# Kernel optimization log

Hardware: AMD Instinct MI355X
Metric: run time of the kernel (lower is better)

Reference implementation:

```python
import jax, jax.numpy as jnp
import numpy as np

DIM = 1024
HEADS = 16
DIM_HEAD = 64
NUM_KV_HEADS = 4
INNER = HEADS * DIM_HEAD          # 1024
KV_DIM = NUM_KV_HEADS * DIM_HEAD  # 256
SCALE = DIM_HEAD ** -0.5


def setup_inputs() -> dict:
    key = jax.random.key(0)
    ks = jax.random.split(key, 7)
    B, S = 2, 2048
    x = jax.random.normal(ks[0], (B, S, DIM), dtype=jnp.float32)
    init = lambda k, shape: jax.random.normal(k, shape, dtype=jnp.float32) * (shape[0] ** -0.5)
    return {
        "x": x,
        "ln_gamma": jnp.ones((DIM,), jnp.float32),
        "ln_beta": jnp.zeros((DIM,), jnp.float32),
        "w_q": init(ks[1], (DIM, INNER)),
        "w_k": init(ks[2], (DIM, KV_DIM)),
        "w_v": init(ks[3], (DIM, KV_DIM)),
        "w_o": init(ks[4], (INNER, DIM)),
        "b_o": jnp.zeros((DIM,), jnp.float32),
    }


def reference(x, ln_gamma, ln_beta, w_q, w_k, w_v, w_o, b_o):
    B, S, _ = x.shape
    g, hpg, d = NUM_KV_HEADS, HEADS // NUM_KV_HEADS, DIM_HEAD
    # LayerNorm (eps matches torch default 1e-5)
    mu = jnp.mean(x, axis=-1, keepdims=True)
    var = jnp.mean((x - mu) ** 2, axis=-1, keepdims=True)
    xn = (x - mu) * jax.lax.rsqrt(var + 1e-5) * ln_gamma + ln_beta
    # projections
    q = xn @ w_q  # [B,S,INNER]
    k = xn @ w_k  # [B,S,KV_DIM]
    v = xn @ w_v
    # q: b s (g hpg d) -> b g hpg s d  (head index h = g*hpg + i, g-major)
    q = q.reshape(B, S, g, hpg, d).transpose(0, 2, 3, 1, 4)
    k = k.reshape(B, S, g, d).transpose(0, 2, 1, 3)  # [B,g,S,d]
    v = v.reshape(B, S, g, d).transpose(0, 2, 1, 3)
    dots = jnp.einsum('bghqd,bgkd->bghqk', q, k) * SCALE
    attn = jax.nn.softmax(dots, axis=-1)
    out = jnp.einsum('bghqk,bgkd->bghqd', attn, v)
    # b g hpg s d -> b s (g hpg d)
    out = out.transpose(0, 3, 1, 2, 4).reshape(B, S, INNER)
    return out @ w_o + b_o
```

## Files before the change

kernel.cpp:

```cpp
#include <hip/hip_runtime.h>

typedef unsigned short u16;
typedef __bf16 bf16x8 __attribute__((ext_vector_type(8)));
typedef short s16x4 __attribute__((ext_vector_type(4)));
typedef float f32x4 __attribute__((ext_vector_type(4)));

__device__ __forceinline__ unsigned f2u(float f) { union { float f; unsigned u; } v; v.f = f; return v.u; }
__device__ __forceinline__ float u2f(unsigned u) { union { unsigned u; float f; } v; v.u = u; return v.f; }

__device__ __forceinline__ u16 f32_to_bf16(float f) {
  unsigned u = f2u(f);
  return (u16)((u + 0x7FFFu + ((u >> 16) & 1u)) >> 16);
}
__device__ __forceinline__ unsigned pack_rnd(float a, float b) {
  unsigned ra = f2u(a), rb = f2u(b);
  ra = ra + 0x7FFFu + ((ra >> 16) & 1u);
  rb = (rb + 0x7FFFu + ((rb >> 16) & 1u)) & 0xFFFF0000u;
  return (ra >> 16) | rb;
}
__device__ __forceinline__ unsigned pack_trunc(float a, float b) {
#if __has_builtin(__builtin_amdgcn_perm)
  return __builtin_amdgcn_perm(f2u(b), f2u(a), 0x07060302u);
#else
  return (f2u(a) >> 16) | (f2u(b) & 0xFFFF0000u);
#endif
}
__device__ __forceinline__ unsigned perm_lo(unsigned a, unsigned b) {
#if __has_builtin(__builtin_amdgcn_perm)
  return __builtin_amdgcn_perm(b, a, 0x05040100u);
#else
  return (a & 0xFFFFu) | (b << 16);
#endif
}
__device__ __forceinline__ unsigned perm_hi(unsigned a, unsigned b) {
#if __has_builtin(__builtin_amdgcn_perm)
  return __builtin_amdgcn_perm(b, a, 0x07060302u);
#else
  return (a >> 16) | (b & 0xFFFF0000u);
#endif
}

__global__ __launch_bounds__(256) void transpose_cvt_multi(
    const float* __restrict__ w_q, const float* __restrict__ w_k,
    const float* __restrict__ w_v, const float* __restrict__ w_o,
    u16* __restrict__ wqkvT, u16* __restrict__ woT) {
  const float* src; u16* dst; int N;
  switch (blockIdx.z) {
    case 0: src = w_q; dst = wqkvT; N = 1024; break;
    case 1: src = w_k; dst = wqkvT + 1024 * 1024; N = 256; break;
    case 2: src = w_v; dst = wqkvT + 1280 * 1024; N = 256; break;
    default: src = w_o; dst = woT; N = 1024; break;
  }
  int n0 = blockIdx.x * 64;
  if (n0 >= N) return;
  const int K = 1024;
  __shared__ float tile[64][65];
  int k0 = blockIdx.y * 64;
  int t = threadIdx.x;
  int c = t & 63, r4 = t >> 6;
#pragma unroll
  for (int rr = r4; rr < 64; rr += 4)
    tile[rr][c] = src[(size_t)(k0 + rr) * N + n0 + c];
  __syncthreads();
#pragma unroll
  for (int rr = r4; rr < 64; rr += 4)
    dst[(size_t)(n0 + rr) * K + k0 + c] = f32_to_bf16(tile[c][rr]);
}

__global__ __launch_bounds__(256) void ln_kernel(
    const float* __restrict__ x, const float* __restrict__ gamma,
    const float* __restrict__ beta, u16* __restrict__ xn) {
  int row = blockIdx.x;
  int t = threadIdx.x;
  const float4 v = ((const float4*)(x + (size_t)row * 1024))[t];
  float s = v.x + v.y + v.z + v.w;
  float ss = v.x * v.x + v.y * v.y + v.z * v.z + v.w * v.w;
#pragma unroll
  for (int m = 1; m < 64; m <<= 1) {
    s += __shfl_xor(s, m, 64);
    ss += __shfl_xor(ss, m, 64);
  }
  __shared__ float as_[4], ass[4];
  int wave = t >> 6;
  if ((t & 63) == 0) { as_[wave] = s; ass[wave] = ss; }
  __syncthreads();
  s = as_[0] + as_[1] + as_[2] + as_[3];
  ss = ass[0] + ass[1] + ass[2] + ass[3];
  float mu = s * (1.0f / 1024.0f);
  float var = ss * (1.0f / 1024.0f) - mu * mu;
  float rstd = rsqrtf(var + 1e-5f);
  float4 g = ((const float4*)gamma)[t];
  float4 b = ((const float4*)beta)[t];
  uint2 o;
  o.x = pack_rnd((v.x - mu) * rstd * g.x + b.x, (v.y - mu) * rstd * g.y + b.y);
  o.y = pack_rnd((v.z - mu) * rstd * g.z + b.z, (v.w - mu) * rstd * g.w + b.w);
  ((uint2*)(xn + (size_t)row * 1024))[t] = o;
}

template <int OUT_MODE>
__global__ __launch_bounds__(256) void gemm_bf16_k(
    const u16* __restrict__ A, const u16* __restrict__ Bt,
    void* __restrict__ Cv, const float* __restrict__ bias,
    int M, int N, int K, int ldc, float qscale, int qcols) {
  __shared__ __align__(16) u16 sA[64 * 72];
  __shared__ __align__(16) u16 sB[128 * 72];
  int t = threadIdx.x;
  int m0 = blockIdx.y * 64, n0 = blockIdx.x * 128;
  int wave = t >> 6, lane = t & 63;
  int wm = wave >> 1, wn = wave & 1;
  int l15 = lane & 15, quad = lane >> 4;

  f32x4 acc[2][4];
#pragma unroll
  for (int i = 0; i < 2; i++)
#pragma unroll
    for (int j = 0; j < 4; j++) acc[i][j] = f32x4{0.f, 0.f, 0.f, 0.f};

  int r = t >> 3, q = t & 7;
  const u16* Ap = A + (size_t)(m0 + r) * K + q * 8;
  const u16* Bp = Bt + (size_t)(n0 + r) * K + q * 8;

  for (int k0 = 0; k0 < K; k0 += 64) {
    uint4 av0 = *(const uint4*)(Ap + k0);
    uint4 av1 = *(const uint4*)(Ap + k0 + (size_t)32 * K);
    uint4 bv0 = *(const uint4*)(Bp + k0);
    uint4 bv1 = *(const uint4*)(Bp + k0 + (size_t)32 * K);
    uint4 bv2 = *(const uint4*)(Bp + k0 + (size_t)64 * K);
    uint4 bv3 = *(const uint4*)(Bp + k0 + (size_t)96 * K);
    __syncthreads();
    *(uint4*)&sA[(r) * 72 + q * 8] = av0;
    *(uint4*)&sA[(r + 32) * 72 + q * 8] = av1;
    *(uint4*)&sB[(r) * 72 + q * 8] = bv0;
    *(uint4*)&sB[(r + 32) * 72 + q * 8] = bv1;
    *(uint4*)&sB[(r + 64) * 72 + q * 8] = bv2;
    *(uint4*)&sB[(r + 96) * 72 + q * 8] = bv3;
    __syncthreads();
#pragma unroll
    for (int ks = 0; ks < 2; ++ks) {
      bf16x8 af[2], bf[4];
#pragma unroll
      for (int mi = 0; mi < 2; mi++)
        af[mi] = *(const bf16x8*)&sA[(wm * 32 + mi * 16 + l15) * 72 + ks * 32 + quad * 8];
#pragma unroll
      for (int ni = 0; ni < 4; ni++)
        bf[ni] = *(const bf16x8*)&sB[(wn * 64 + ni * 16 + l15) * 72 + ks * 32 + quad * 8];
#pragma unroll
      for (int mi = 0; mi < 2; mi++)
#pragma unroll
        for (int ni = 0; ni < 4; ni++)
          acc[mi][ni] = __builtin_amdgcn_mfma_f32_16x16x32_bf16(
              af[mi], bf[ni], acc[mi][ni], 0, 0, 0);
    }
  }
#pragma unroll
  for (int mi = 0; mi < 2; mi++)
#pragma unroll
    for (int ni = 0; ni < 4; ni++) {
      int row = m0 + wm * 32 + mi * 16 + quad * 4;
      int col = n0 + wn * 64 + ni * 16 + l15;
#pragma unroll
      for (int rr = 0; rr < 4; rr++) {
        float vv = acc[mi][ni][rr];
        if (OUT_MODE == 0) {
          float sc = (col < qcols) ? qscale : 1.0f;
          ((u16*)Cv)[(size_t)(row + rr) * ldc + col] = f32_to_bf16(vv * sc);
        } else {
          ((float*)Cv)[(size_t)(row + rr) * ldc + col] = vv + bias[col];
        }
      }
    }
}

__global__ __launch_bounds__(256) void attn_kernel(
    const u16* __restrict__ qkv, u16* __restrict__ oP0, u16* __restrict__ oP1,
    float* __restrict__ lP0, float* __restrict__ lP1) {
  const int LD = 1536;
  int qt = blockIdx.x;
  int bh = blockIdx.y;
  int kz = blockIdx.z;
  int b = bh >> 4, h = bh & 15, g = h >> 2;
  u16* oP = kz ? oP1 : oP0;
  float* lP = kz ? lP1 : lP0;

  __shared__ __align__(16) u16 sK[64 * 72];
  __shared__ __align__(16) u16 sV[64 * 72];

  int t = threadIdx.x, wave = t >> 6, lane = t & 63;
  int l15 = lane & 15, quad = lane >> 4;

  const u16* qbase = qkv + (size_t)(b * 2048 + qt * 256 + wave * 64) * LD + h * 64;
  const u16* kbase = qkv + (size_t)(b * 2048 + kz * 1024) * LD + 1024 + g * 64;
  const u16* vbase = kbase + 256;

  bf16x8 qf[4][2];
#pragma unroll
  for (int qs = 0; qs < 4; ++qs)
#pragma unroll
    for (int ks = 0; ks < 2; ++ks)
      qf[qs][ks] = *(const bf16x8*)(qbase + (size_t)(qs * 16 + l15) * LD + ks * 32 + quad * 8);

  f32x4 oacc[4][4];
  f32x4 lacc[4];
#pragma unroll
  for (int qs = 0; qs < 4; ++qs) {
    lacc[qs] = f32x4{0.f, 0.f, 0.f, 0.f};
#pragma unroll
    for (int md = 0; md < 4; ++md) oacc[qs][md] = f32x4{0.f, 0.f, 0.f, 0.f};
  }

  const s16x4 ones = {(short)0x3F80, (short)0x3F80, (short)0x3F80, (short)0x3F80};
  const f32x4 fzero = {0.f, 0.f, 0.f, 0.f};

  int sr = t >> 3, sq = t & 7;
  int vkp = (t & 31) * 2, vdc = (t >> 5) * 8;

  uint4 ka0, ka1, va0, va1;
  {
    const u16* kp0 = kbase + (size_t)sr * LD + sq * 8;
    ka0 = *(const uint4*)kp0;
    ka1 = *(const uint4*)(kp0 + (size_t)32 * LD);
    const u16* vp0 = vbase + (size_t)vkp * LD + vdc;
    va0 = *(const uint4*)vp0;
    va1 = *(const uint4*)(vp0 + LD);
  }

  for (int kt = 0; kt < 16; ++kt) {
    __syncthreads();
    *(uint4*)&sK[sr * 72 + sq * 8] = ka0;
    *(uint4*)&sK[(sr + 32) * 72 + sq * 8] = ka1;
    {
      const unsigned* aw = (const unsigned*)&va0;
      const unsigned* bw = (const unsigned*)&va1;
#pragma unroll
      for (int w = 0; w < 4; ++w) {
        *(unsigned*)&sV[(vdc + 2 * w) * 72 + vkp] = perm_lo(aw[w], bw[w]);
        *(unsigned*)&sV[(vdc + 2 * w + 1) * 72 + vkp] = perm_hi(aw[w], bw[w]);
      }
    }
    __syncthreads();

    if (kt < 15) {
      const u16* kp0 = kbase + (size_t)((kt + 1) * 64 + sr) * LD + sq * 8;
      ka0 = *(const uint4*)kp0;
      ka1 = *(const uint4*)(kp0 + (size_t)32 * LD);
      const u16* vp0 = vbase + (size_t)((kt + 1) * 64 + vkp) * LD + vdc;
      va0 = *(const uint4*)vp0;
      va1 = *(const uint4*)(vp0 + LD);
    }

    s16x4 pf[4][4];
#pragma unroll
    for (int ni = 0; ni < 4; ++ni) {
      bf16x8 kf0 = *(const bf16x8*)&sK[(ni * 16 + l15) * 72 + quad * 8];
      bf16x8 kf1 = *(const bf16x8*)&sK[(ni * 16 + l15) * 72 + 32 + quad * 8];
      f32x4 sacc[4];
#pragma unroll
      for (int qs = 0; qs < 4; ++qs)
        sacc[qs] = __builtin_amdgcn_mfma_f32_16x16x32_bf16(kf0, qf[qs][0], fzero, 0, 0, 0);
#pragma unroll
      for (int qs = 0; qs < 4; ++qs)
        sacc[qs] = __builtin_amdgcn_mfma_f32_16x16x32_bf16(kf1, qf[qs][1], sacc[qs], 0, 0, 0);
#pragma unroll
      for (int qs = 0; qs < 4; ++qs) {
        float p0 = __builtin_amdgcn_exp2f(sacc[qs][0]);
        float p1 = __builtin_amdgcn_exp2f(sacc[qs][1]);
        float p2 = __builtin_amdgcn_exp2f(sacc[qs][2]);
        float p3 = __builtin_amdgcn_exp2f(sacc[qs][3]);
        uint2 pk;
        pk.x = pack_trunc(p0, p1);
        pk.y = pack_trunc(p2, p3);
        pf[qs][ni] = *(s16x4*)&pk;
        lacc[qs] = __builtin_amdgcn_mfma_f32_16x16x16bf16_1k(ones, pf[qs][ni], lacc[qs], 0, 0, 0);
      }
    }

#pragma unroll
    for (int md = 0; md < 4; ++md)
#pragma unroll
      for (int ni = 0; ni < 4; ++ni) {
        s16x4 vf = *(const s16x4*)&sV[(md * 16 + l15) * 72 + ni * 16 + quad * 4];
#pragma unroll
        for (int qs = 0; qs < 4; ++qs)
          oacc[qs][md] = __builtin_amdgcn_mfma_f32_16x16x16bf16_1k(vf, pf[qs][ni], oacc[qs][md], 0, 0, 0);
      }
  }

#pragma unroll
  for (int qs = 0; qs < 4; ++qs) {
    int row = b * 2048 + qt * 256 + wave * 64 + qs * 16 + l15;
    u16* ob = oP + (size_t)row * 1024 + h * 64 + quad * 4;
#pragma unroll
    for (int md = 0; md < 4; ++md) {
      uint2 o;
      o.x = pack_rnd(oacc[qs][md][0], oacc[qs][md][1]);
      o.y = pack_rnd(oacc[qs][md][2], oacc[qs][md][3]);
      *(uint2*)(ob + md * 16) = o;
    }
    if (quad == 0) lP[row * 16 + h] = lacc[qs][0];
  }
}

__global__ __launch_bounds__(256) void attn_combine(
    const u16* __restrict__ oP0, u16* __restrict__ oP1_attn,
    const float* __restrict__ lP0, const float* __restrict__ lP1) {
  int t = threadIdx.x;
  int row = blockIdx.x * 2 + (t >> 7);
  int c8 = (t & 127) * 8;
  int h = c8 >> 6;
  float l = lP0[row * 16 + h] + lP1[row * 16 + h];
  float rinv = 1.0f / l;
  size_t off = (size_t)row * 1024 + c8;
  uint4 a = *(const uint4*)(oP0 + off);
  uint4 bb = *(const uint4*)(oP1_attn + off);
  const unsigned* aw = (const unsigned*)&a;
  const unsigned* bw = (const unsigned*)&bb;
  uint4 o;
  unsigned* ow = (unsigned*)&o;
#pragma unroll
  for (int i = 0; i < 4; ++i) {
    float x0 = u2f(aw[i] << 16) + u2f(bw[i] << 16);
    float x1 = u2f(aw[i] & 0xFFFF0000u) + u2f(bw[i] & 0xFFFF0000u);
    ow[i] = pack_rnd(x0 * rinv, x1 * rinv);
  }
  *(uint4*)(oP1_attn + off) = o;
}

extern "C" void kernel_launch(void* const* d_in, const int* in_sizes, int n_in,
                              void* d_out, int out_size, void* d_ws, size_t ws_size,
                              hipStream_t stream) {
  const float* x = (const float*)d_in[0];
  const float* gamma = (const float*)d_in[1];
  const float* beta = (const float*)d_in[2];
  const float* w_q = (const float*)d_in[3];
  const float* w_k = (const float*)d_in[4];
  const float* w_v = (const float*)d_in[5];
  const float* w_o = (const float*)d_in[6];
  const float* b_o = (const float*)d_in[7];
  float* out = (float*)d_out;

  char* ws = (char*)d_ws;
  u16* wqkvT = (u16*)ws;
  float* lP0 = (float*)ws;
  float* lP1 = (float*)(ws + 256u * 1024);
  u16* woT = (u16*)(ws + 3u * 1024 * 1024);
  u16* xn = (u16*)(ws + 5u * 1024 * 1024);
  u16* oP0 = xn;
  u16* qkv = (u16*)(ws + 13u * 1024 * 1024);
  u16* oP1 = (u16*)(ws + 25u * 1024 * 1024);

  const float cexp = 0.125f * 1.44269504088896f;

  transpose_cvt_multi<<<dim3(16, 16, 4), 256, 0, stream>>>(w_q, w_k, w_v, w_o,
                                                           wqkvT, woT);
  ln_kernel<<<4096, 256, 0, stream>>>(x, gamma, beta, xn);

  gemm_bf16_k<0><<<dim3(12, 64), 256, 0, stream>>>(xn, wqkvT, qkv, nullptr,
                                                   4096, 1536, 1024, 1536,
                                                   cexp, 1024);

  attn_kernel<<<dim3(8, 32, 2), 256, 0, stream>>>(qkv, oP0, oP1, lP0, lP1);
  attn_combine<<<dim3(2048), 256, 0, stream>>>(oP0, oP1, lP0, lP1);

  gemm_bf16_k<1><<<dim3(8, 64), 256, 0, stream>>>(oP1, woT, out, b_o,
                                                  4096, 1024, 1024, 1024,
                                                  1.0f, 0);
}
```

Before: 187.3 us.

## Switch attention inner loops to 32x32x16 bf16 MFMA tiles

Rewrites the attention kernel's QK^T, PV and row-sum accumulation to use 32x32x16 bf16 MFMA instructions instead of 16x16 variants. The P fragments produced by the score MFMA feed the PV MFMA directly, and the V tile is stored to shared memory with a permuted key-column index so its layout matches the 32x32 operand layout. The aim is fewer MFMA issues and fewer LDS fragment loads per tile. In exchange it needs larger accumulator register sets (f32x16), which raises register pressure and may lower occupancy.

```diff
diff --git a/kernel.cpp b/kernel.cpp
--- a/kernel.cpp
+++ b/kernel.cpp
@@ -4,6 +4,7 @@
 typedef __bf16 bf16x8 __attribute__((ext_vector_type(8)));
 typedef short s16x4 __attribute__((ext_vector_type(4)));
 typedef float f32x4 __attribute__((ext_vector_type(4)));
+typedef float f32x16 __attribute__((ext_vector_type(16)));
 
 __device__ __forceinline__ unsigned f2u(float f) { union { float f; unsigned u; } v; v.f = f; return v.u; }
 __device__ __forceinline__ float u2f(unsigned u) { union { unsigned u; float f; } v; v.u = u; return v.f; }
@@ -186,33 +187,35 @@
   __shared__ __align__(16) u16 sV[64 * 72];
 
   int t = threadIdx.x, wave = t >> 6, lane = t & 63;
-  int l15 = lane & 15, quad = lane >> 4;
+  int l31 = lane & 31, hh = lane >> 5;
 
   const u16* qbase = qkv + (size_t)(b * 2048 + qt * 256 + wave * 64) * LD + h * 64;
   const u16* kbase = qkv + (size_t)(b * 2048 + kz * 1024) * LD + 1024 + g * 64;
   const u16* vbase = kbase + 256;
 
-  bf16x8 qf[4][2];
-#pragma unroll
-  for (int qs = 0; qs < 4; ++qs)
-#pragma unroll
-    for (int ks = 0; ks < 2; ++ks)
-      qf[qs][ks] = *(const bf16x8*)(qbase + (size_t)(qs * 16 + l15) * LD + ks * 32 + quad * 8);
-
-  f32x4 oacc[4][4];
-  f32x4 lacc[4];
-#pragma unroll
-  for (int qs = 0; qs < 4; ++qs) {
-    lacc[qs] = f32x4{0.f, 0.f, 0.f, 0.f};
-#pragma unroll
-    for (int md = 0; md < 4; ++md) oacc[qs][md] = f32x4{0.f, 0.f, 0.f, 0.f};
-  }
-
-  const s16x4 ones = {(short)0x3F80, (short)0x3F80, (short)0x3F80, (short)0x3F80};
-  const f32x4 fzero = {0.f, 0.f, 0.f, 0.f};
+  bf16x8 qf[2][4];
+#pragma unroll
+  for (int q2 = 0; q2 < 2; ++q2)
+#pragma unroll
+    for (int ds = 0; ds < 4; ++ds)
+      qf[q2][ds] = *(const bf16x8*)(qbase + (size_t)(q2 * 32 + l31) * LD + ds * 16 + hh * 8);
+
+  f32x16 oacc[2][2];
+  f32x16 lacc[2];
+#pragma unroll
+  for (int i = 0; i < 16; ++i) {
+    oacc[0][0][i] = 0.f; oacc[0][1][i] = 0.f;
+    oacc[1][0][i] = 0.f; oacc[1][1][i] = 0.f;
+    lacc[0][i] = 0.f; lacc[1][i] = 0.f;
+  }
+  union { u16 s[8]; bf16x8 v; } vones;
+#pragma unroll
+  for (int i = 0; i < 8; ++i) vones.s[i] = 0x3F80;
 
   int sr = t >> 3, sq = t & 7;
   int vkp = (t & 31) * 2, vdc = (t >> 5) * 8;
+  int x = vkp & 15;
+  int vc = (vkp & ~15) | (x & 3) | ((x & 4) << 1) | ((x & 8) >> 1);
 
   uint4 ka0, ka1, va0, va1;
   {
@@ -233,8 +236,8 @@
       const unsigned* bw = (const unsigned*)&va1;
 #pragma unroll
       for (int w = 0; w < 4; ++w) {
-        *(unsigned*)&sV[(vdc + 2 * w) * 72 + vkp] = perm_lo(aw[w], bw[w]);
-        *(unsigned*)&sV[(vdc + 2 * w + 1) * 72 + vkp] = perm_hi(aw[w], bw[w]);
+        *(unsigned*)&sV[(vdc + 2 * w) * 72 + vc] = perm_lo(aw[w], bw[w]);
+        *(unsigned*)&sV[(vdc + 2 * w + 1) * 72 + vc] = perm_hi(aw[w], bw[w]);
       }
     }
     __syncthreads();
@@ -248,55 +251,69 @@
       va1 = *(const uint4*)(vp0 + LD);
     }
 
-    s16x4 pf[4][4];
-#pragma unroll
-    for (int ni = 0; ni < 4; ++ni) {
-      bf16x8 kf0 = *(const bf16x8*)&sK[(ni * 16 + l15) * 72 + quad * 8];
-      bf16x8 kf1 = *(const bf16x8*)&sK[(ni * 16 + l15) * 72 + 32 + quad * 8];
-      f32x4 sacc[4];
-#pragma unroll
-      for (int qs = 0; qs < 4; ++qs)
-        sacc[qs] = __builtin_amdgcn_mfma_f32_16x16x32_bf16(kf0, qf[qs][0], fzero, 0, 0, 0);
-#pragma unroll
-      for (int qs = 0; qs < 4; ++qs)
-        sacc[qs] = __builtin_amdgcn_mfma_f32_16x16x32_bf16(kf1, qf[qs][1], sacc[qs], 0, 0, 0);
-#pragma unroll
-      for (int qs = 0; qs < 4; ++qs) {
-        float p0 = __builtin_amdgcn_exp2f(sacc[qs][0]);
-        float p1 = __builtin_amdgcn_exp2f(sacc[qs][1]);
-        float p2 = __builtin_amdgcn_exp2f(sacc[qs][2]);
-        float p3 = __builtin_amdgcn_exp2f(sacc[qs][3]);
-        uint2 pk;
-        pk.x = pack_trunc(p0, p1);
-        pk.y = pack_trunc(p2, p3);
-        pf[qs][ni] = *(s16x4*)&pk;
-        lacc[qs] = __builtin_amdgcn_mfma_f32_16x16x16bf16_1k(ones, pf[qs][ni], lacc[qs], 0, 0, 0);
-      }
-    }
-
-#pragma unroll
-    for (int md = 0; md < 4; ++md)
-#pragma unroll
-      for (int ni = 0; ni < 4; ++ni) {
-        s16x4 vf = *(const s16x4*)&sV[(md * 16 + l15) * 72 + ni * 16 + quad * 4];
-#pragma unroll
-        for (int qs = 0; qs < 4; ++qs)
-          oacc[qs][md] = __builtin_amdgcn_mfma_f32_16x16x16bf16_1k(vf, pf[qs][ni], oacc[qs][md], 0, 0, 0);
-      }
-  }
-
-#pragma unroll
-  for (int qs = 0; qs < 4; ++qs) {
-    int row = b * 2048 + qt * 256 + wave * 64 + qs * 16 + l15;
-    u16* ob = oP + (size_t)row * 1024 + h * 64 + quad * 4;
-#pragma unroll
-    for (int md = 0; md < 4; ++md) {
-      uint2 o;
-      o.x = pack_rnd(oacc[qs][md][0], oacc[qs][md][1]);
-      o.y = pack_rnd(oacc[qs][md][2], oacc[qs][md][3]);
-      *(uint2*)(ob + md * 16) = o;
-    }
-    if (quad == 0) lP[row * 16 + h] = lacc[qs][0];
+#pragma unroll
+    for (int ktile = 0; ktile < 2; ++ktile) {
+      bf16x8 kf[4];
+#pragma unroll
+      for (int ds = 0; ds < 4; ++ds)
+        kf[ds] = *(const bf16x8*)&sK[(ktile * 32 + l31) * 72 + ds * 16 + hh * 8];
+
+      union { unsigned u[4]; bf16x8 v; } pb[2][2];
+#pragma unroll
+      for (int q2 = 0; q2 < 2; ++q2) {
+        f32x16 sc;
+#pragma unroll
+        for (int i = 0; i < 16; ++i) sc[i] = 0.f;
+#pragma unroll
+        for (int ds = 0; ds < 4; ++ds)
+          sc = __builtin_amdgcn_mfma_f32_32x32x16_bf16(kf[ds], qf[q2][ds], sc, 0, 0, 0);
+        unsigned p[8];
+#pragma unroll
+        for (int i = 0; i < 8; ++i) {
+          float e0 = __builtin_amdgcn_exp2f(sc[2 * i]);
+          float e1 = __builtin_amdgcn_exp2f(sc[2 * i + 1]);
+          p[i] = pack_trunc(e0, e1);
+        }
+        pb[q2][0].u[0] = p[0]; pb[q2][0].u[1] = p[1];
+        pb[q2][0].u[2] = p[2]; pb[q2][0].u[3] = p[3];
+        pb[q2][1].u[0] = p[4]; pb[q2][1].u[1] = p[5];
+        pb[q2][1].u[2] = p[6]; pb[q2][1].u[3] = p[7];
+      }
+
+#pragma unroll
+      for (int u = 0; u < 2; ++u) {
+        int s = ktile * 2 + u;
+#pragma unroll
+        for (int dt = 0; dt < 2; ++dt) {
+          bf16x8 vf = *(const bf16x8*)&sV[(dt * 32 + l31) * 72 + s * 16 + hh * 8];
+#pragma unroll
+          for (int q2 = 0; q2 < 2; ++q2)
+            oacc[q2][dt] = __builtin_amdgcn_mfma_f32_32x32x16_bf16(
+                vf, pb[q2][u].v, oacc[q2][dt], 0, 0, 0);
+        }
+#pragma unroll
+        for (int q2 = 0; q2 < 2; ++q2)
+          lacc[q2] = __builtin_amdgcn_mfma_f32_32x32x16_bf16(
+              vones.v, pb[q2][u].v, lacc[q2], 0, 0, 0);
+      }
+    }
+  }
+
+#pragma unroll
+  for (int q2 = 0; q2 < 2; ++q2) {
+    int row = b * 2048 + qt * 256 + wave * 64 + q2 * 32 + l31;
+    if (hh == 0) lP[row * 16 + h] = lacc[q2][0];
+    u16* ob = oP + (size_t)row * 1024 + h * 64;
+#pragma unroll
+    for (int dt = 0; dt < 2; ++dt)
+#pragma unroll
+      for (int rg = 0; rg < 4; ++rg) {
+        int d0 = dt * 32 + 8 * rg + 4 * hh;
+        uint2 o;
+        o.x = pack_rnd(oacc[q2][dt][4 * rg], oacc[q2][dt][4 * rg + 1]);
+        o.y = pack_rnd(oacc[q2][dt][4 * rg + 2], oacc[q2][dt][4 * rg + 3]);
+        *(uint2*)(ob + d0) = o;
+      }
   }
 }
 
```

Result: slower. 202.6 us (+8.2%).

## Use async global-to-LDS loads in GEMM and fuse LayerNorm with weight prep

Applied to the files above, without the earlier changes.

The GEMM tile staging now uses global_load_lds direct copies into an unpadded 64-stride LDS layout instead of loading into registers and storing to LDS. The LayerNorm and weight transpose/convert kernels are merged into a single launch partitioned by block index. This is meant to cut register traffic and launch overhead. Removing the LDS padding may introduce bank conflicts on fragment reads.

```diff
diff --git a/kernel.cpp b/kernel.cpp
--- a/kernel.cpp
+++ b/kernel.cpp
@@ -40,23 +40,68 @@
 #endif
 }
 
-__global__ __launch_bounds__(256) void transpose_cvt_multi(
+#if __has_builtin(__builtin_amdgcn_global_load_lds)
+#define ASYNC_CP 1
+typedef __attribute__((address_space(1))) const unsigned gu32;
+typedef __attribute__((address_space(3))) unsigned lu32;
+__device__ __forceinline__ void gl_lds16(const u16* g, u16* l) {
+  __builtin_amdgcn_global_load_lds((gu32*)g, (lu32*)l, 16, 0, 0);
+}
+#else
+#define ASYNC_CP 0
+#endif
+
+__global__ __launch_bounds__(256) void prep_kernel(
+    const float* __restrict__ x, const float* __restrict__ gamma,
+    const float* __restrict__ beta, u16* __restrict__ xn,
     const float* __restrict__ w_q, const float* __restrict__ w_k,
     const float* __restrict__ w_v, const float* __restrict__ w_o,
     u16* __restrict__ wqkvT, u16* __restrict__ woT) {
-  const float* src; u16* dst; int N;
-  switch (blockIdx.z) {
-    case 0: src = w_q; dst = wqkvT; N = 1024; break;
-    case 1: src = w_k; dst = wqkvT + 1024 * 1024; N = 256; break;
-    case 2: src = w_v; dst = wqkvT + 1280 * 1024; N = 256; break;
-    default: src = w_o; dst = woT; N = 1024; break;
-  }
-  int n0 = blockIdx.x * 64;
-  if (n0 >= N) return;
+  __shared__ float tile[64][65];
+  int t = threadIdx.x;
+  int bid = blockIdx.x;
+  if (bid < 4096) {
+    int row = bid;
+    const float4 v = ((const float4*)(x + (size_t)row * 1024))[t];
+    float s = v.x + v.y + v.z + v.w;
+    float ss = v.x * v.x + v.y * v.y + v.z * v.z + v.w * v.w;
+#pragma unroll
+    for (int m = 1; m < 64; m <<= 1) {
+      s += __shfl_xor(s, m, 64);
+      ss += __shfl_xor(ss, m, 64);
+    }
+    __shared__ float as_[4], ass[4];
+    int wave = t >> 6;
+    if ((t & 63) == 0) { as_[wave] = s; ass[wave] = ss; }
+    __syncthreads();
+    s = as_[0] + as_[1] + as_[2] + as_[3];
+    ss = ass[0] + ass[1] + ass[2] + ass[3];
+    float mu = s * (1.0f / 1024.0f);
+    float var = ss * (1.0f / 1024.0f) - mu * mu;
+    float rstd = rsqrtf(var + 1e-5f);
+    float4 g = ((const float4*)gamma)[t];
+    float4 b = ((const float4*)beta)[t];
+    uint2 o;
+    o.x = pack_rnd((v.x - mu) * rstd * g.x + b.x, (v.y - mu) * rstd * g.y + b.y);
+    o.y = pack_rnd((v.z - mu) * rstd * g.z + b.z, (v.w - mu) * rstd * g.w + b.w);
+    ((uint2*)(xn + (size_t)row * 1024))[t] = o;
+    return;
+  }
+  int idx = bid - 4096;
+  const float* src; u16* dst; int N, n0, k0;
+  if (idx < 256) {
+    src = w_q; dst = wqkvT; N = 1024; n0 = (idx & 15) * 64; k0 = (idx >> 4) * 64;
+  } else if (idx < 320) {
+    int i = idx - 256;
+    src = w_k; dst = wqkvT + 1024 * 1024; N = 256; n0 = (i & 3) * 64; k0 = (i >> 2) * 64;
+  } else if (idx < 384) {
+    int i = idx - 320;
+    src = w_v; dst = wqkvT + 1280 * 1024; N = 256; n0 = (i & 3) * 64; k0 = (i >> 2) * 64;
+  } else {
+    int i = idx - 384;
+    src = w_o; dst = woT; N = 1024; n0 = (i & 15) * 64; k0 = (i >> 4) * 64;
+  }
   const int K = 1024;
-  __shared__ float tile[64][65];
-  int k0 = blockIdx.y * 64;
-  int t = threadIdx.x;
   int c = t & 63, r4 = t >> 6;
 #pragma unroll
   for (int rr = r4; rr < 64; rr += 4)
@@ -65,36 +110,6 @@
 #pragma unroll
   for (int rr = r4; rr < 64; rr += 4)
     dst[(size_t)(n0 + rr) * K + k0 + c] = f32_to_bf16(tile[c][rr]);
-}
-
-__global__ __launch_bounds__(256) void ln_kernel(
-    const float* __restrict__ x, const float* __restrict__ gamma,
-    const float* __restrict__ beta, u16* __restrict__ xn) {
-  int row = blockIdx.x;
-  int t = threadIdx.x;
-  const float4 v = ((const float4*)(x + (size_t)row * 1024))[t];
-  float s = v.x + v.y + v.z + v.w;
-  float ss = v.x * v.x + v.y * v.y + v.z * v.z + v.w * v.w;
-#pragma unroll
-  for (int m = 1; m < 64; m <<= 1) {
-    s += __shfl_xor(s, m, 64);
-    ss += __shfl_xor(ss, m, 64);
-  }
-  __shared__ float as_[4], ass[4];
-  int wave = t >> 6;
-  if ((t & 63) == 0) { as_[wave] = s; ass[wave] = ss; }
-  __syncthreads();
-  s = as_[0] + as_[1] + as_[2] + as_[3];
-  ss = ass[0] + ass[1] + ass[2] + ass[3];
-  float mu = s * (1.0f / 1024.0f);
-  float var = ss * (1.0f / 1024.0f) - mu * mu;
-  float rstd = rsqrtf(var + 1e-5f);
-  float4 g = ((const float4*)gamma)[t];
-  float4 b = ((const float4*)beta)[t];
-  uint2 o;
-  o.x = pack_rnd((v.x - mu) * rstd * g.x + b.x, (v.y - mu) * rstd * g.y + b.y);
-  o.y = pack_rnd((v.z - mu) * rstd * g.z + b.z, (v.w - mu) * rstd * g.w + b.w);
-  ((uint2*)(xn + (size_t)row * 1024))[t] = o;
 }
 
 template <int OUT_MODE>
@@ -102,8 +117,8 @@
     const u16* __restrict__ A, const u16* __restrict__ Bt,
     void* __restrict__ Cv, const float* __restrict__ bias,
     int M, int N, int K, int ldc, float qscale, int qcols) {
-  __shared__ __align__(16) u16 sA[64 * 72];
-  __shared__ __align__(16) u16 sB[128 * 72];
+  __shared__ __align__(16) u16 sA[64 * 64];
+  __shared__ __align__(16) u16 sB[128 * 64];
   int t = threadIdx.x;
   int m0 = blockIdx.y * 64, n0 = blockIdx.x * 128;
   int wave = t >> 6, lane = t & 63;
@@ -116,11 +131,24 @@
 #pragma unroll
     for (int j = 0; j < 4; j++) acc[i][j] = f32x4{0.f, 0.f, 0.f, 0.f};
 
-  int r = t >> 3, q = t & 7;
-  const u16* Ap = A + (size_t)(m0 + r) * K + q * 8;
-  const u16* Bp = Bt + (size_t)(n0 + r) * K + q * 8;
+  int arow = wave * 8 + (lane >> 3);
+  int achk = (lane & 7) * 8;
+  const u16* Ap = A + (size_t)(m0 + arow) * K + achk;
+  const u16* Bp = Bt + (size_t)(n0 + arow) * K + achk;
+  u16* sAw = &sA[(wave * 8) * 64];
+  u16* sBw = &sB[(wave * 8) * 64];
 
   for (int k0 = 0; k0 < K; k0 += 64) {
+#if ASYNC_CP
+    __syncthreads();
+    gl_lds16(Ap + k0, sAw);
+    gl_lds16(Ap + k0 + (size_t)32 * K, sAw + 32 * 64);
+    gl_lds16(Bp + k0, sBw);
+    gl_lds16(Bp + k0 + (size_t)32 * K, sBw + 32 * 64);
+    gl_lds16(Bp + k0 + (size_t)64 * K, sBw + 64 * 64);
+    gl_lds16(Bp + k0 + (size_t)96 * K, sBw + 96 * 64);
+    __syncthreads();
+#else
     uint4 av0 = *(const uint4*)(Ap + k0);
     uint4 av1 = *(const uint4*)(Ap + k0 + (size_t)32 * K);
     uint4 bv0 = *(const uint4*)(Bp + k0);
@@ -128,22 +156,23 @@
     uint4 bv2 = *(const uint4*)(Bp + k0 + (size_t)64 * K);
     uint4 bv3 = *(const uint4*)(Bp + k0 + (size_t)96 * K);
     __syncthreads();
-    *(uint4*)&sA[(r) * 72 + q * 8] = av0;
-    *(uint4*)&sA[(r + 32) * 72 + q * 8] = av1;
-    *(uint4*)&sB[(r) * 72 + q * 8] = bv0;
-    *(uint4*)&sB[(r + 32) * 72 + q * 8] = bv1;
-    *(uint4*)&sB[(r + 64) * 72 + q * 8] = bv2;
-    *(uint4*)&sB[(r + 96) * 72 + q * 8] = bv3;
-    __syncthreads();
+    *(uint4*)&sA[arow * 64 + achk] = av0;
+    *(uint4*)&sA[(arow + 32) * 64 + achk] = av1;
+    *(uint4*)&sB[arow * 64 + achk] = bv0;
+    *(uint4*)&sB[(arow + 32) * 64 + achk] = bv1;
+    *(uint4*)&sB[(arow + 64) * 64 + achk] = bv2;
+    *(uint4*)&sB[(arow + 96) * 64 + achk] = bv3;
+    __syncthreads();
+#endif
 #pragma unroll
     for (int ks = 0; ks < 2; ++ks) {
       bf16x8 af[2], bf[4];
 #pragma unroll
       for (int mi = 0; mi < 2; mi++)
-        af[mi] = *(const bf16x8*)&sA[(wm * 32 + mi * 16 + l15) * 72 + ks * 32 + quad * 8];
+        af[mi] = *(const bf16x8*)&sA[(wm * 32 + mi * 16 + l15) * 64 + ks * 32 + quad * 8];
 #pragma unroll
       for (int ni = 0; ni < 4; ni++)
-        bf[ni] = *(const bf16x8*)&sB[(wn * 64 + ni * 16 + l15) * 72 + ks * 32 + quad * 8];
+        bf[ni] = *(const bf16x8*)&sB[(wn * 64 + ni * 16 + l15) * 64 + ks * 32 + quad * 8];
 #pragma unroll
       for (int mi = 0; mi < 2; mi++)
 #pragma unroll
@@ -350,9 +379,8 @@
 
   const float cexp = 0.125f * 1.44269504088896f;
 
-  transpose_cvt_multi<<<dim3(16, 16, 4), 256, 0, stream>>>(w_q, w_k, w_v, w_o,
-                                                           wqkvT, woT);
-  ln_kernel<<<4096, 256, 0, stream>>>(x, gamma, beta, xn);
+  prep_kernel<<<4736, 256, 0, stream>>>(x, gamma, beta, xn, w_q, w_k, w_v, w_o,
+                                        wqkvT, woT);
 
   gemm_bf16_k<0><<<dim3(12, 64), 256, 0, stream>>>(xn, wqkvT, qkv, nullptr,
                                                    4096, 1536, 1024, 1536,
```

Measured after the change: 189.3 us. About the same (+1.1%).
